# Optimization experiments

Hardware: AMD Instinct MI355X
Metric: run time of the kernel (lower is better)

Reference implementation:

```python
import jax, jax.numpy as jnp
import numpy as np

K_SCHEDULE = (4, 8, 16)


def setup_inputs() -> dict:
    key = jax.random.key(0)
    B, T, D = 2, 2048, 1024
    R = len(K_SCHEDULE)
    kx, = jax.random.split(key, 1)
    return {
        "x": jax.random.normal(kx, (B, T, D), dtype=jnp.float32),
        "gain": jnp.ones((R, D), dtype=jnp.float32),
        "bias": jnp.zeros((R, D), dtype=jnp.float32),
        "log_mix": jnp.zeros((R,), dtype=jnp.float32),
        "log_momentum": jnp.asarray(1.0, dtype=jnp.float32),
        "log_scale": jnp.asarray(0.0, dtype=jnp.float32),
    }


def _round(h, K, gain_r, bias_r, mix, momentum):
    B, T, D = h.shape
    # causal top-K adjacency from evolving hidden state
    scores = jnp.einsum("bid,bjd->bij", h, h)                      # (B,T,T)
    causal = jnp.tril(jnp.ones((T, T), dtype=bool))                # j <= i
    masked = jnp.where(causal[None], scores, -jnp.inf)
    vals, idx = jax.lax.top_k(masked, K)                           # (B,T,K)
    valid = jnp.isfinite(vals)                                     # early rows have < K causal neighbors
    # unweighted (mean) neighbor aggregation via gather
    gathered = jnp.take_along_axis(h[:, None, :, :], idx[..., None], axis=2)  # (B,T,K,D)
    vf = valid.astype(h.dtype)
    count = jnp.maximum(vf.sum(-1, keepdims=True), 1.0)            # (B,T,1)
    msg = (gathered * vf[..., None]).sum(axis=2) / count           # (B,T,D)
    # gated residual blend + affine + GELU + momentum update
    blended = mix * h + (1.0 - mix) * msg
    h_new = jax.nn.gelu(blended * gain_r + bias_r, approximate=False)
    return momentum * h + (1.0 - momentum) * h_new


def reference(x, gain, bias, log_mix, log_momentum, log_scale):
    momentum = jax.nn.sigmoid(log_momentum)
    scale = jax.nn.softplus(log_scale) + 0.01
    h = x
    for r, K_r in enumerate(K_SCHEDULE):
        mix = jax.nn.sigmoid(log_mix[r])
        h = _round(h, K_r, gain[r], bias[r], mix, momentum)
    return (h - x) * scale
```

## Files before the change

kernel.cpp:

```cpp
#include <hip/hip_runtime.h>
#include <math.h>

#define BB 2
#define TT 2048
#define DD 1024
#define NTHREADS 256

#define RT 64
#define CT 128
#define DC 32
#define NCHUNK (DD / DC)
#define NJC (TT / CT)
#define KMAX 16
#define CST 132
#define NTILES 272
#define NROWS (BB * TT)
#define CSLAB ((uint32_t)(NROWS * DC))
#define PLANE ((uint32_t)(BB * TT * DD))
#define HBUF 12288


typedef _Float16 half8  __attribute__((ext_vector_type(8)));
typedef _Float16 half4v __attribute__((ext_vector_type(4)));
typedef float    float4v __attribute__((ext_vector_type(4)));

#define GLD16(gp, lp) __builtin_amdgcn_global_load_lds(                         \
    (const __attribute__((address_space(1))) unsigned int*)(gp),                \
    (__attribute__((address_space(3))) unsigned int*)(lp), 16, 0, 0)

__device__ __forceinline__ float gelu_exact(float t) {
    return 0.5f * t * (1.0f + erff(t * 0.70710678118654752f));
}

__global__ __launch_bounds__(NTHREADS) void split_kernel(
    const float* __restrict__ h,
    _Float16* __restrict__ hiP,
    _Float16* __restrict__ loP)
{
    const int idx = blockIdx.x * NTHREADS + threadIdx.x;
    const float4 v = ((const float4*)h)[idx];
    const float xs[4] = {v.x, v.y, v.z, v.w};
    half4v hi, lo;
    #pragma unroll
    for (int u = 0; u < 4; ++u) {
        const _Float16 hh = (_Float16)xs[u];
        hi[u] = hh;
        lo[u] = (_Float16)(xs[u] - (float)hh);
    }
    const uint32_t tot  = (uint32_t)idx * 4u;
    const uint32_t grow = tot >> 10;
    const uint32_t wh   = tot & 1023u;
    const uint32_t off  = ((wh >> 5) * (uint32_t)NROWS + grow) * 32u + (wh & 31u);
    *(half4v*)(hiP + off) = hi;
    *(half4v*)(loP + off) = lo;
}

__global__ __launch_bounds__(NTHREADS) void score_topk_kernel(
    const _Float16* __restrict__ hiP,
    float* __restrict__ pval,
    int*   __restrict__ pidx,
    int K)
{
    __shared__ __align__(16) char smem_raw[49152];
    _Float16* sm  = (_Float16*)smem_raw;
    float* scores = (float*)smem_raw;

    const int b = blockIdx.y;
    const int p = blockIdx.x;
    int g = (int)(0.5f * (sqrtf(4.0f * (float)p + 1.0f) - 1.0f));
    while ((g + 1) * (g + 2) <= p) ++g;
    while (g * (g + 1) > p) --g;
    const int qq = p - g * (g + 1);
    const int it = 2 * g + qq / (g + 1);
    const int jc = qq % (g + 1);
    const int i0 = it * RT, j0 = jc * CT;

    const int tid  = threadIdx.x;
    const int lane = tid & 63, wave = tid >> 6;
    const int wr = wave & 1, wc = wave >> 1;

    uint32_t goff[6];
    #pragma unroll
    for (int slot = 0; slot < 6; ++slot) {
        const int gr = tid + NTHREADS * slot;
        int n, row; uint32_t pl;
        if (gr < 256)       { n = gr;        pl = 0; row = i0 + 16 * (n >> 6) + (n & 15); }
        else if (gr < 512)  { n = gr - 256;  pl = 1; row = i0 + 16 * (n >> 6) + (n & 15); }
        else if (gr < 1024) { n = gr - 512;  pl = 0; row = j0 + 16 * (n >> 6) + (n & 15); }
        else                { n = gr - 1024; pl = 1; row = j0 + 16 * (n >> 6) + (n & 15); }
        const int oct = (n >> 4) & 3;
        goff[slot] = pl * PLANE + (uint32_t)(b * TT + row) * DC + (uint32_t)oct * 8;
    }

    float4v acc[2][4];
    #pragma unroll
    for (int rb = 0; rb < 2; ++rb)
        #pragma unroll
        for (int cb = 0; cb < 4; ++cb)
            acc[rb][cb] = (float4v){0.f, 0.f, 0.f, 0.f};

    #pragma unroll
    for (int t = 0; t < 6; ++t)
        GLD16(hiP + goff[t], &sm[(size_t)(tid + NTHREADS * t) * 8]);
    #pragma unroll
    for (int t = 0; t < 6; ++t)
        GLD16(hiP + goff[t] + CSLAB, &sm[HBUF + (size_t)(tid + NTHREADS * t) * 8]);

    for (int c = 0; c < NCHUNK; ++c) {
        const int cur = (c & 1) ? HBUF : 0;

        if (c < NCHUNK - 1) asm volatile("s_waitcnt vmcnt(6)" ::: "memory");
        else                asm volatile("s_waitcnt vmcnt(0)" ::: "memory");
        __builtin_amdgcn_s_barrier();
        asm volatile("" ::: "memory");

        half8 ah[2], al[2], bh[4], bl[4];
        #pragma unroll
        for (int rb = 0; rb < 2; ++rb) {
            const int band = 2 * wr + rb;
            ah[rb] = *(const half8*)&sm[cur +        (band * 64 + lane) * 8];
            al[rb] = *(const half8*)&sm[cur + 2048 + (band * 64 + lane) * 8];
        }
        #pragma unroll
        for (int cb = 0; cb < 4; ++cb) {
            const int band = 4 * wc + cb;
            bh[cb] = *(const half8*)&sm[cur + 4096 + (band * 64 + lane) * 8];
            bl[cb] = *(const half8*)&sm[cur + 8192 + (band * 64 + lane) * 8];
        }

        asm volatile("s_waitcnt lgkmcnt(0)" ::: "memory");
        __builtin_amdgcn_s_barrier();
        asm volatile("" ::: "memory");

        if (c + 2 < NCHUNK) {
            #pragma unroll
            for (int t = 0; t < 6; ++t)
                GLD16(hiP + goff[t] + (uint32_t)(c + 2) * CSLAB,
                      &sm[cur + (size_t)(tid + NTHREADS * t) * 8]);
        }
        __builtin_amdgcn_sched_barrier(0);

        __builtin_amdgcn_s_setprio(1);
        #pragma unroll
        for (int rb = 0; rb < 2; ++rb)
            #pragma unroll
            for (int cb = 0; cb < 4; ++cb) {
                acc[rb][cb] = __builtin_amdgcn_mfma_f32_16x16x32_f16(ah[rb], bh[cb], acc[rb][cb], 0, 0, 0);
                acc[rb][cb] = __builtin_amdgcn_mfma_f32_16x16x32_f16(ah[rb], bl[cb], acc[rb][cb], 0, 0, 0);
                acc[rb][cb] = __builtin_amdgcn_mfma_f32_16x16x32_f16(al[rb], bh[cb], acc[rb][cb], 0, 0, 0);
            }
        __builtin_amdgcn_s_setprio(0);
    }

    {
        const int qn = lane >> 4, rn = lane & 15;
        #pragma unroll
        for (int rb = 0; rb < 2; ++rb)
            #pragma unroll
            for (int cb = 0; cb < 4; ++cb)
                #pragma unroll
                for (int reg = 0; reg < 4; ++reg) {
                    const int i_loc = 32 * wr + 16 * rb + qn * 4 + reg;
                    const int j_loc = 64 * wc + 16 * cb + rn;
                    scores[i_loc * CST + j_loc] =
                        (j0 + j_loc <= i0 + i_loc) ? acc[rb][cb][reg] : -INFINITY;
                }
    }
    __syncthreads();

    const int rloc = tid >> 2, seg = tid & 3;
    const float* Crow = scores + rloc * CST;
    float vals[32];
    #pragma unroll
    for (int cc = 0; cc < 32; ++cc) vals[cc] = Crow[seg + 4 * cc];

    uint32_t dead = 0;
    const int irow = i0 + rloc;
    const size_t obase = ((size_t)(b * TT + irow) * NJC + jc) * KMAX;
    for (int k = 0; k < K; ++k) {
        float bv = -INFINITY; int bcc = -1;
        #pragma unroll
        for (int cc = 0; cc < 32; ++cc) {
            const bool alive = ((dead >> cc) & 1u) == 0u;
            if (alive && vals[cc] > bv) { bv = vals[cc]; bcc = cc; }
        }
        const int bcol = (bcc >= 0) ? (seg + 4 * bcc) : -1;
        float wv = bv; int wcol = bcol;
        #pragma unroll
        for (int m = 1; m < 4; m <<= 1) {
            const float ov = __shfl_xor(wv, m, 64);
            const int   oc = __shfl_xor(wcol, m, 64);
            if (ov > wv || (ov == wv && (unsigned)oc < (unsigned)wcol)) { wv = ov; wcol = oc; }
        }
        if (seg == 0) {
            pval[obase + k] = wv;
            pidx[obase + k] = (wcol >= 0) ? (j0 + wcol) : -1;
        }
        if (bcc >= 0 && wcol == bcol) dead |= (1u << bcc);
    }
}

template<int K>
__global__ __launch_bounds__(NTHREADS) void merge_agg_kernel(
    const float* __restrict__ h_in,
    float* __restrict__ h_out,
    const float* __restrict__ pval,
    const int*   __restrict__ pidx,
    const float* __restrict__ gain,
    const float* __restrict__ bias,
    const float* __restrict__ log_mix_r,
    const float* __restrict__ log_momentum,
    const float* __restrict__ xres,
    const float* __restrict__ log_scale,
    _Float16* __restrict__ hiO,
    _Float16* __restrict__ loO)
{
    constexpr int KL = (K == 4) ? 2 : (K == 8) ? 3 : 4;
    __shared__ __align__(16) float s_cval[NTHREADS];
    __shared__ __align__(16) int   s_cidx[NTHREADS];
    __shared__ int s_sel[KMAX];

    const int row = blockIdx.x, b = row / TT, i = row % TT;
    const int tid = threadIdx.x;
    const float* hb = h_in + (size_t)b * TT * DD;

    const int count = (i + 1 < K) ? (i + 1) : K;
    const int jcn = i / CT + 1;
    const int ncand = jcn * K;

    float mv = -INFINITY; int mj = -1;
    if (tid < ncand) {
        const int w = tid >> KL, k = tid & (K - 1);
        const size_t base = ((size_t)(b * TT + i) * NJC + w) * KMAX + k;
        const int j = pidx[base];
        if (j >= 0) { mj = j; mv = pval[base]; }
    }
    s_cval[tid] = mv;
    s_cidx[tid] = mj;

    const float4 hi = ((const float4*)(hb + (size_t)i * DD))[tid];
    const float4 g4 = ((const float4*)gain)[tid];
    const float4 c4 = ((const float4*)bias)[tid];
    __syncthreads();

    if (mj >= 0) {
        const int nb = (ncand + 3) >> 2;
        int rank = 0;
        for (int q = 0; q < nb; ++q) {
            const float4 v4 = ((const float4*)s_cval)[q];
            const int4  j4 = ((const int4*)s_cidx)[q];
            rank += (v4.x > mv || (v4.x == mv && (unsigned)j4.x < (unsigned)mj));
            rank += (v4.y > mv || (v4.y == mv && (unsigned)j4.y < (unsigned)mj));
            rank += (v4.z > mv || (v4.z == mv && (unsigned)j4.z < (unsigned)mj));
            rank += (v4.w > mv || (v4.w == mv && (unsigned)j4.w < (unsigned)mj));
        }
        if (rank < count) s_sel[rank] = mj;
    }
    __syncthreads();

    const float mix      = 1.0f / (1.0f + expf(-log_mix_r[0]));
    const float momentum = 1.0f / (1.0f + expf(-log_momentum[0]));
    const float inv_cnt  = 1.0f / (float)count;

    float4 msg = make_float4(0.f, 0.f, 0.f, 0.f);
    if (count == K) {
        #pragma unroll
        for (int k = 0; k < K; ++k) {
            const float4 v = ((const float4*)(hb + (size_t)s_sel[k] * DD))[tid];
            msg.x += v.x; msg.y += v.y; msg.z += v.z; msg.w += v.w;
        }
    } else {
        for (int k = 0; k < count; ++k) {
            const float4 v = ((const float4*)(hb + (size_t)s_sel[k] * DD))[tid];
            msg.x += v.x; msg.y += v.y; msg.z += v.z; msg.w += v.w;
        }
    }

    float4 o;
    {
        float m, t;
        m = msg.x * inv_cnt; t = (mix * hi.x + (1.f - mix) * m) * g4.x + c4.x;
        o.x = momentum * hi.x + (1.f - momentum) * gelu_exact(t);
        m = msg.y * inv_cnt; t = (mix * hi.y + (1.f - mix) * m) * g4.y + c4.y;
        o.y = momentum * hi.y + (1.f - momentum) * gelu_exact(t);
        m = msg.z * inv_cnt; t = (mix * hi.z + (1.f - mix) * m) * g4.z + c4.z;
        o.z = momentum * hi.z + (1.f - momentum) * gelu_exact(t);
        m = msg.w * inv_cnt; t = (mix * hi.w + (1.f - mix) * m) * g4.w + c4.w;
        o.w = momentum * hi.w + (1.f - momentum) * gelu_exact(t);
    }

    if (hiO != nullptr) {
        const float os[4] = {o.x, o.y, o.z, o.w};
        half4v hv, lv;
        #pragma unroll
        for (int u = 0; u < 4; ++u) {
            const _Float16 hh = (_Float16)os[u];
            hv[u] = hh;
            lv[u] = (_Float16)(os[u] - (float)hh);
        }
        const uint32_t wh  = (uint32_t)tid * 4u;
        const uint32_t off = ((wh >> 5) * (uint32_t)NROWS + (uint32_t)row) * 32u + (wh & 31u);
        *(half4v*)(hiO + off) = hv;
        *(half4v*)(loO + off) = lv;
    }

    if (xres != nullptr) {
        const float scale = log1pf(expf(log_scale[0])) + 0.01f;
        const float4 xv = ((const float4*)(xres + (size_t)row * DD))[tid];
        o.x = (o.x - xv.x) * scale;
        o.y = (o.y - xv.y) * scale;
        o.z = (o.z - xv.z) * scale;
        o.w = (o.w - xv.w) * scale;
    }
    ((float4*)(h_out + (size_t)row * DD))[tid] = o;
}

extern "C" void kernel_launch(void* const* d_in, const int* in_sizes, int n_in,
                              void* d_out, int out_size, void* d_ws, size_t ws_size,
                              hipStream_t stream) {
    const float* x            = (const float*)d_in[0];
    const float* gain         = (const float*)d_in[1];
    const float* bias         = (const float*)d_in[2];
    const float* log_mix      = (const float*)d_in[3];
    const float* log_momentum = (const float*)d_in[4];
    const float* log_scale    = (const float*)d_in[5];
    float* out = (float*)d_out;

    char* wsb = (char*)d_ws;
    float*     h_ws = (float*)wsb;
    float*     pval = (float*)(wsb + (size_t)BB * TT * DD * 4);
    int*       pidx = (int*)  (wsb + (size_t)BB * TT * DD * 4 + (size_t)BB * TT * NJC * KMAX * 4);
    _Float16*  hiP  = (_Float16*)(wsb + (size_t)BB * TT * DD * 4 + (size_t)BB * TT * NJC * KMAX * 8);
    _Float16*  loP  = hiP + (size_t)PLANE;

    const dim3 sgrid(NTILES, BB);
    const int nsplit = BB * TT * DD / 4 / NTHREADS;

    split_kernel<<<nsplit, NTHREADS, 0, stream>>>(x, hiP, loP);
    score_topk_kernel<<<sgrid, NTHREADS, 0, stream>>>(hiP, pval, pidx, 4);
    merge_agg_kernel<4><<<BB * TT, NTHREADS, 0, stream>>>(
        x, out, pval, pidx, gain + 0 * DD, bias + 0 * DD, log_mix + 0, log_momentum,
        nullptr, nullptr, hiP, loP);
    score_topk_kernel<<<sgrid, NTHREADS, 0, stream>>>(hiP, pval, pidx, 8);
    merge_agg_kernel<8><<<BB * TT, NTHREADS, 0, stream>>>(
        out, h_ws, pval, pidx, gain + 1 * DD, bias + 1 * DD, log_mix + 1, log_momentum,
        nullptr, nullptr, hiP, loP);
    score_topk_kernel<<<sgrid, NTHREADS, 0, stream>>>(hiP, pval, pidx, 16);
    merge_agg_kernel<16><<<BB * TT, NTHREADS, 0, stream>>>(
        h_ws, out, pval, pidx, gain + 2 * DD, bias + 2 * DD, log_mix + 2, log_momentum,
        x, log_scale, nullptr, nullptr);
}
```

Baseline: 301.0 us.

## Triple-buffer LDS chunks in score kernel to drop one barrier per chunk

Switches the score GEMM's LDS staging from two buffers to three and unrolls the chunk loop by three. The prefetch for chunk c+2 can then go into a third buffer right after the first barrier, which removes the second per-chunk barrier that used to protect buffer reuse. In exchange, LDS use grows from 48KB to 72KB per block, which may cut the number of resident blocks per CU and so reduce occupancy. A final syncthreads is added before the scores reuse the shared memory.

```diff
diff --git a/kernel.cpp b/kernel.cpp
--- a/kernel.cpp
+++ b/kernel.cpp
@@ -17,7 +17,9 @@
 #define NROWS (BB * TT)
 #define CSLAB ((uint32_t)(NROWS * DC))
 #define PLANE ((uint32_t)(BB * TT * DD))
-#define HBUF 12288
+#define B0 0
+#define B1 12288
+#define B2 24576
 
 
 typedef _Float16 half8  __attribute__((ext_vector_type(8)));
@@ -61,7 +63,7 @@
     int*   __restrict__ pidx,
     int K)
 {
-    __shared__ __align__(16) char smem_raw[49152];
+    __shared__ __align__(16) char smem_raw[73728];
     _Float16* sm  = (_Float16*)smem_raw;
     float* scores = (float*)smem_raw;
 
@@ -101,56 +103,62 @@
 
     #pragma unroll
     for (int t = 0; t < 6; ++t)
-        GLD16(hiP + goff[t], &sm[(size_t)(tid + NTHREADS * t) * 8]);
+        GLD16(hiP + goff[t], &sm[B0 + (size_t)(tid + NTHREADS * t) * 8]);
     #pragma unroll
     for (int t = 0; t < 6; ++t)
-        GLD16(hiP + goff[t] + CSLAB, &sm[HBUF + (size_t)(tid + NTHREADS * t) * 8]);
-
-    for (int c = 0; c < NCHUNK; ++c) {
-        const int cur = (c & 1) ? HBUF : 0;
-
-        if (c < NCHUNK - 1) asm volatile("s_waitcnt vmcnt(6)" ::: "memory");
-        else                asm volatile("s_waitcnt vmcnt(0)" ::: "memory");
-        __builtin_amdgcn_s_barrier();
-        asm volatile("" ::: "memory");
-
-        half8 ah[2], al[2], bh[4], bl[4];
-        #pragma unroll
-        for (int rb = 0; rb < 2; ++rb) {
-            const int band = 2 * wr + rb;
-            ah[rb] = *(const half8*)&sm[cur +        (band * 64 + lane) * 8];
-            al[rb] = *(const half8*)&sm[cur + 2048 + (band * 64 + lane) * 8];
-        }
-        #pragma unroll
-        for (int cb = 0; cb < 4; ++cb) {
-            const int band = 4 * wc + cb;
-            bh[cb] = *(const half8*)&sm[cur + 4096 + (band * 64 + lane) * 8];
-            bl[cb] = *(const half8*)&sm[cur + 8192 + (band * 64 + lane) * 8];
-        }
-
-        asm volatile("s_waitcnt lgkmcnt(0)" ::: "memory");
-        __builtin_amdgcn_s_barrier();
-        asm volatile("" ::: "memory");
-
-        if (c + 2 < NCHUNK) {
-            #pragma unroll
-            for (int t = 0; t < 6; ++t)
-                GLD16(hiP + goff[t] + (uint32_t)(c + 2) * CSLAB,
-                      &sm[cur + (size_t)(tid + NTHREADS * t) * 8]);
-        }
-        __builtin_amdgcn_sched_barrier(0);
-
-        __builtin_amdgcn_s_setprio(1);
-        #pragma unroll
-        for (int rb = 0; rb < 2; ++rb)
-            #pragma unroll
-            for (int cb = 0; cb < 4; ++cb) {
-                acc[rb][cb] = __builtin_amdgcn_mfma_f32_16x16x32_f16(ah[rb], bh[cb], acc[rb][cb], 0, 0, 0);
-                acc[rb][cb] = __builtin_amdgcn_mfma_f32_16x16x32_f16(ah[rb], bl[cb], acc[rb][cb], 0, 0, 0);
-                acc[rb][cb] = __builtin_amdgcn_mfma_f32_16x16x32_f16(al[rb], bh[cb], acc[rb][cb], 0, 0, 0);
-            }
-        __builtin_amdgcn_s_setprio(0);
-    }
+        GLD16(hiP + goff[t] + CSLAB, &sm[B1 + (size_t)(tid + NTHREADS * t) * 8]);
+
+#define CHUNK1B(c, BCUR, BNXT, VMSTR, DO_ISSUE) do {                              \
+        asm volatile("s_waitcnt vmcnt(" VMSTR ")" ::: "memory");                  \
+        __builtin_amdgcn_s_barrier();                                             \
+        asm volatile("" ::: "memory");                                            \
+        if (DO_ISSUE) {                                                           \
+            _Pragma("unroll")                                                     \
+            for (int t = 0; t < 6; ++t)                                           \
+                GLD16(hiP + goff[t] + (uint32_t)((c) + 2) * CSLAB,                \
+                      &sm[(BNXT) + (size_t)(tid + NTHREADS * t) * 8]);            \
+        }                                                                         \
+        __builtin_amdgcn_sched_barrier(0);                                        \
+        half8 ah[2], al[2], bh[4], bl[4];                                         \
+        _Pragma("unroll")                                                         \
+        for (int rb = 0; rb < 2; ++rb) {                                          \
+            const int band = 2 * wr + rb;                                         \
+            ah[rb] = *(const half8*)&sm[(BCUR) +        (band * 64 + lane) * 8];  \
+            al[rb] = *(const half8*)&sm[(BCUR) + 2048 + (band * 64 + lane) * 8];  \
+        }                                                                         \
+        _Pragma("unroll")                                                         \
+        for (int cb = 0; cb < 4; ++cb) {                                          \
+            const int band = 4 * wc + cb;                                         \
+            bh[cb] = *(const half8*)&sm[(BCUR) + 4096 + (band * 64 + lane) * 8];  \
+            bl[cb] = *(const half8*)&sm[(BCUR) + 8192 + (band * 64 + lane) * 8];  \
+        }                                                                         \
+        asm volatile("s_waitcnt lgkmcnt(0)" ::: "memory");                        \
+        __builtin_amdgcn_sched_barrier(0);                                        \
+        __builtin_amdgcn_s_setprio(1);                                            \
+        _Pragma("unroll")                                                         \
+        for (int rb = 0; rb < 2; ++rb)                                            \
+            _Pragma("unroll")                                                     \
+            for (int cb = 0; cb < 4; ++cb) {                                      \
+                acc[rb][cb] = __builtin_amdgcn_mfma_f32_16x16x32_f16(             \
+                    ah[rb], bh[cb], acc[rb][cb], 0, 0, 0);                        \
+                acc[rb][cb] = __builtin_amdgcn_mfma_f32_16x16x32_f16(             \
+                    ah[rb], bl[cb], acc[rb][cb], 0, 0, 0);                        \
+                acc[rb][cb] = __builtin_amdgcn_mfma_f32_16x16x32_f16(             \
+                    al[rb], bh[cb], acc[rb][cb], 0, 0, 0);                        \
+            }                                                                     \
+        __builtin_amdgcn_s_setprio(0);                                            \
+    } while (0)
+
+    for (int ct = 0; ct < 10; ++ct) {
+        CHUNK1B(3 * ct + 0, B0, B2, "6", 1);
+        CHUNK1B(3 * ct + 1, B1, B0, "6", 1);
+        CHUNK1B(3 * ct + 2, B2, B1, "6", 1);
+    }
+    CHUNK1B(30, B0, B2, "6", 0);
+    CHUNK1B(31, B1, B0, "0", 0);
+#undef CHUNK1B
+
+    __syncthreads();
 
     {
         const int qn = lane >> 4, rn = lane & 15;
```

New measurement: 311.2 us. 1.03x slower.

## Software-pipeline LDS fragment loads against MFMA with register double-buffering

Applied to the files above, without the earlier changes.

Restructures the score GEMM main loop so that the LDS fragments for the next K-chunk are read into a second register set while the MFMAs for the current chunk run. This needs only one barrier per chunk instead of two. The loop is unrolled by two with explicit even and odd fragment sets. Launch bounds now request 3 blocks per CU to cap register use. The doubled fragment registers plus the occupancy hint risk spills, and the wait is now vmcnt(0) each step instead of vmcnt(6), which can expose global load latency.

```diff
diff --git a/kernel.cpp b/kernel.cpp
--- a/kernel.cpp
+++ b/kernel.cpp
@@ -55,7 +55,7 @@
     *(half4v*)(loP + off) = lo;
 }
 
-__global__ __launch_bounds__(NTHREADS) void score_topk_kernel(
+__global__ __launch_bounds__(NTHREADS, 3) void score_topk_kernel(
     const _Float16* __restrict__ hiP,
     float* __restrict__ pval,
     int*   __restrict__ pidx,
@@ -99,58 +99,85 @@
         for (int cb = 0; cb < 4; ++cb)
             acc[rb][cb] = (float4v){0.f, 0.f, 0.f, 0.f};
 
+    half8 ahE[2], alE[2], bhE[4], blE[4];
+    half8 ahO[2], alO[2], bhO[4], blO[4];
+
+#define LDFRAG(AH, AL, BH, BL, BASE) do {                                        \
+        _Pragma("unroll")                                                        \
+        for (int rb = 0; rb < 2; ++rb) {                                         \
+            const int band = 2 * wr + rb;                                        \
+            AH[rb] = *(const half8*)&sm[(BASE) +        (band * 64 + lane) * 8]; \
+            AL[rb] = *(const half8*)&sm[(BASE) + 2048 + (band * 64 + lane) * 8]; \
+        }                                                                        \
+        _Pragma("unroll")                                                        \
+        for (int cb = 0; cb < 4; ++cb) {                                         \
+            const int band = 4 * wc + cb;                                        \
+            BH[cb] = *(const half8*)&sm[(BASE) + 4096 + (band * 64 + lane) * 8]; \
+            BL[cb] = *(const half8*)&sm[(BASE) + 8192 + (band * 64 + lane) * 8]; \
+        }                                                                        \
+    } while (0)
+
+#define DOMFMA(AH, AL, BH, BL) do {                                              \
+        __builtin_amdgcn_s_setprio(1);                                           \
+        _Pragma("unroll")                                                        \
+        for (int rb = 0; rb < 2; ++rb)                                           \
+            _Pragma("unroll")                                                    \
+            for (int cb = 0; cb < 4; ++cb) {                                     \
+                acc[rb][cb] = __builtin_amdgcn_mfma_f32_16x16x32_f16(            \
+                    AH[rb], BH[cb], acc[rb][cb], 0, 0, 0);                       \
+                acc[rb][cb] = __builtin_amdgcn_mfma_f32_16x16x32_f16(            \
+                    AH[rb], BL[cb], acc[rb][cb], 0, 0, 0);                       \
+                acc[rb][cb] = __builtin_amdgcn_mfma_f32_16x16x32_f16(            \
+                    AL[rb], BH[cb], acc[rb][cb], 0, 0, 0);                       \
+            }                                                                    \
+        __builtin_amdgcn_s_setprio(0);                                           \
+    } while (0)
+
+#define PIPE(BCUR, BNXT, FaH, FaL, FbH, FbL, NaH, NaL, NbH, NbL, DO_DMA)         \
+    do {                                                                         \
+        asm volatile("s_waitcnt lgkmcnt(0)" ::: "memory");                       \
+        asm volatile("s_waitcnt vmcnt(0)"  ::: "memory");                        \
+        __builtin_amdgcn_s_barrier();                                            \
+        __builtin_amdgcn_sched_barrier(0);                                       \
+        if (DO_DMA) {                                                            \
+            _Pragma("unroll")                                                    \
+            for (int t = 0; t < 6; ++t)                                          \
+                GLD16(hiP + goff[t] + coff,                                      \
+                      &sm[(BCUR) + (size_t)(tid + NTHREADS * t) * 8]);           \
+            coff += (uint32_t)CSLAB;                                             \
+        }                                                                        \
+        __builtin_amdgcn_sched_barrier(0);                                       \
+        LDFRAG(NaH, NaL, NbH, NbL, BNXT);                                        \
+        __builtin_amdgcn_sched_barrier(0);                                       \
+        DOMFMA(FaH, FaL, FbH, FbL);                                              \
+    } while (0)
+
     #pragma unroll
     for (int t = 0; t < 6; ++t)
         GLD16(hiP + goff[t], &sm[(size_t)(tid + NTHREADS * t) * 8]);
     #pragma unroll
     for (int t = 0; t < 6; ++t)
         GLD16(hiP + goff[t] + CSLAB, &sm[HBUF + (size_t)(tid + NTHREADS * t) * 8]);
-
-    for (int c = 0; c < NCHUNK; ++c) {
-        const int cur = (c & 1) ? HBUF : 0;
-
-        if (c < NCHUNK - 1) asm volatile("s_waitcnt vmcnt(6)" ::: "memory");
-        else                asm volatile("s_waitcnt vmcnt(0)" ::: "memory");
-        __builtin_amdgcn_s_barrier();
-        asm volatile("" ::: "memory");
-
-        half8 ah[2], al[2], bh[4], bl[4];
-        #pragma unroll
-        for (int rb = 0; rb < 2; ++rb) {
-            const int band = 2 * wr + rb;
-            ah[rb] = *(const half8*)&sm[cur +        (band * 64 + lane) * 8];
-            al[rb] = *(const half8*)&sm[cur + 2048 + (band * 64 + lane) * 8];
-        }
-        #pragma unroll
-        for (int cb = 0; cb < 4; ++cb) {
-            const int band = 4 * wc + cb;
-            bh[cb] = *(const half8*)&sm[cur + 4096 + (band * 64 + lane) * 8];
-            bl[cb] = *(const half8*)&sm[cur + 8192 + (band * 64 + lane) * 8];
-        }
-
-        asm volatile("s_waitcnt lgkmcnt(0)" ::: "memory");
-        __builtin_amdgcn_s_barrier();
-        asm volatile("" ::: "memory");
-
-        if (c + 2 < NCHUNK) {
-            #pragma unroll
-            for (int t = 0; t < 6; ++t)
-                GLD16(hiP + goff[t] + (uint32_t)(c + 2) * CSLAB,
-                      &sm[cur + (size_t)(tid + NTHREADS * t) * 8]);
-        }
-        __builtin_amdgcn_sched_barrier(0);
-
-        __builtin_amdgcn_s_setprio(1);
-        #pragma unroll
-        for (int rb = 0; rb < 2; ++rb)
-            #pragma unroll
-            for (int cb = 0; cb < 4; ++cb) {
-                acc[rb][cb] = __builtin_amdgcn_mfma_f32_16x16x32_f16(ah[rb], bh[cb], acc[rb][cb], 0, 0, 0);
-                acc[rb][cb] = __builtin_amdgcn_mfma_f32_16x16x32_f16(ah[rb], bl[cb], acc[rb][cb], 0, 0, 0);
-                acc[rb][cb] = __builtin_amdgcn_mfma_f32_16x16x32_f16(al[rb], bh[cb], acc[rb][cb], 0, 0, 0);
-            }
-        __builtin_amdgcn_s_setprio(0);
-    }
+    asm volatile("s_waitcnt vmcnt(6)" ::: "memory");
+    __builtin_amdgcn_s_barrier();
+    asm volatile("" ::: "memory");
+    LDFRAG(ahE, alE, bhE, blE, 0);
+
+    uint32_t coff = 2u * CSLAB;
+
+    for (int ci = 0; ci < 15; ++ci) {
+        PIPE(0,    HBUF, ahE, alE, bhE, blE, ahO, alO, bhO, blO, 1);
+        PIPE(HBUF, 0,    ahO, alO, bhO, blO, ahE, alE, bhE, blE, 1);
+    }
+    PIPE(0, HBUF, ahE, alE, bhE, blE, ahO, alO, bhO, blO, 0);
+    asm volatile("s_waitcnt lgkmcnt(0)" ::: "memory");
+    __builtin_amdgcn_sched_barrier(0);
+    DOMFMA(ahO, alO, bhO, blO);
+#undef PIPE
+#undef DOMFMA
+#undef LDFRAG
+
+    __syncthreads();
 
     {
         const int qn = lane >> 4, rn = lane & 15;
```

Result: no change. 296.3 us (-1.6%).

## Enlarge score tile to 128x128 with 512-thread blocks

Applied to the files above, without the earlier changes.

The score/top-k kernel now computes square 128x128 tiles of the causal score matrix using 8 waves per block instead of 64x128 tiles with 4 waves. The triangular tile enumeration changes to match, and per-block shared memory grows. The goal is more reuse of each loaded fragment and fewer blocks with redundant loads. In exchange there are fewer, larger blocks, possibly lower occupancy, and more wasted work on diagonal tiles. The top-k epilogue, unchanged in the visible code, must handle 128 score rows with 512 threads.

```diff
diff --git a/kernel.cpp b/kernel.cpp
--- a/kernel.cpp
+++ b/kernel.cpp
@@ -4,20 +4,21 @@
 #define BB 2
 #define TT 2048
 #define DD 1024
-#define NTHREADS 256
-
-#define RT 64
+
+#define RT 128
 #define CT 128
 #define DC 32
 #define NCHUNK (DD / DC)
 #define NJC (TT / CT)
 #define KMAX 16
 #define CST 132
-#define NTILES 272
+#define NT2 136
 #define NROWS (BB * TT)
 #define CSLAB ((uint32_t)(NROWS * DC))
 #define PLANE ((uint32_t)(BB * TT * DD))
-#define HBUF 12288
+#define HBUF 16384
+#define NTH_S 512
+#define NTHREADS 256
 
 
 typedef _Float16 half8  __attribute__((ext_vector_type(8)));
@@ -55,77 +56,75 @@
     *(half4v*)(loP + off) = lo;
 }
 
-__global__ __launch_bounds__(NTHREADS) void score_topk_kernel(
+__global__ __launch_bounds__(NTH_S) void score_topk_kernel(
     const _Float16* __restrict__ hiP,
     float* __restrict__ pval,
     int*   __restrict__ pidx,
     int K)
 {
-    __shared__ __align__(16) char smem_raw[49152];
+    __shared__ __align__(16) char smem_raw[67584];
     _Float16* sm  = (_Float16*)smem_raw;
     float* scores = (float*)smem_raw;
 
     const int b = blockIdx.y;
     const int p = blockIdx.x;
-    int g = (int)(0.5f * (sqrtf(4.0f * (float)p + 1.0f) - 1.0f));
-    while ((g + 1) * (g + 2) <= p) ++g;
-    while (g * (g + 1) > p) --g;
-    const int qq = p - g * (g + 1);
-    const int it = 2 * g + qq / (g + 1);
-    const int jc = qq % (g + 1);
+    int it = (int)((sqrtf(8.0f * (float)p + 1.0f) - 1.0f) * 0.5f);
+    while ((it + 1) * (it + 2) / 2 <= p) ++it;
+    while (it * (it + 1) / 2 > p) --it;
+    const int jc = p - it * (it + 1) / 2;
     const int i0 = it * RT, j0 = jc * CT;
 
     const int tid  = threadIdx.x;
     const int lane = tid & 63, wave = tid >> 6;
     const int wr = wave & 1, wc = wave >> 1;
 
-    uint32_t goff[6];
-    #pragma unroll
-    for (int slot = 0; slot < 6; ++slot) {
-        const int gr = tid + NTHREADS * slot;
-        int n, row; uint32_t pl;
-        if (gr < 256)       { n = gr;        pl = 0; row = i0 + 16 * (n >> 6) + (n & 15); }
-        else if (gr < 512)  { n = gr - 256;  pl = 1; row = i0 + 16 * (n >> 6) + (n & 15); }
-        else if (gr < 1024) { n = gr - 512;  pl = 0; row = j0 + 16 * (n >> 6) + (n & 15); }
-        else                { n = gr - 1024; pl = 1; row = j0 + 16 * (n >> 6) + (n & 15); }
+    uint32_t goff[4];
+    #pragma unroll
+    for (int slot = 0; slot < 4; ++slot) {
+        const int gr = tid + NTH_S * slot;
+        const int region = gr >> 9;
+        const int n = gr & 511;
+        const uint32_t pl = (uint32_t)(region & 1);
+        const int row0 = (region < 2) ? i0 : j0;
+        const int row = row0 + 16 * (n >> 6) + (n & 15);
         const int oct = (n >> 4) & 3;
         goff[slot] = pl * PLANE + (uint32_t)(b * TT + row) * DC + (uint32_t)oct * 8;
     }
 
-    float4v acc[2][4];
-    #pragma unroll
-    for (int rb = 0; rb < 2; ++rb)
-        #pragma unroll
-        for (int cb = 0; cb < 4; ++cb)
+    float4v acc[4][2];
+    #pragma unroll
+    for (int rb = 0; rb < 4; ++rb)
+        #pragma unroll
+        for (int cb = 0; cb < 2; ++cb)
             acc[rb][cb] = (float4v){0.f, 0.f, 0.f, 0.f};
 
     #pragma unroll
-    for (int t = 0; t < 6; ++t)
-        GLD16(hiP + goff[t], &sm[(size_t)(tid + NTHREADS * t) * 8]);
-    #pragma unroll
-    for (int t = 0; t < 6; ++t)
-        GLD16(hiP + goff[t] + CSLAB, &sm[HBUF + (size_t)(tid + NTHREADS * t) * 8]);
+    for (int t = 0; t < 4; ++t)
+        GLD16(hiP + goff[t], &sm[(size_t)(tid + NTH_S * t) * 8]);
+    #pragma unroll
+    for (int t = 0; t < 4; ++t)
+        GLD16(hiP + goff[t] + CSLAB, &sm[HBUF + (size_t)(tid + NTH_S * t) * 8]);
 
     for (int c = 0; c < NCHUNK; ++c) {
         const int cur = (c & 1) ? HBUF : 0;
 
-        if (c < NCHUNK - 1) asm volatile("s_waitcnt vmcnt(6)" ::: "memory");
+        if (c < NCHUNK - 1) asm volatile("s_waitcnt vmcnt(4)" ::: "memory");
         else                asm volatile("s_waitcnt vmcnt(0)" ::: "memory");
         __builtin_amdgcn_s_barrier();
         asm volatile("" ::: "memory");
 
-        half8 ah[2], al[2], bh[4], bl[4];
-        #pragma unroll
-        for (int rb = 0; rb < 2; ++rb) {
-            const int band = 2 * wr + rb;
+        half8 ah[4], al[4], bh[2], bl[2];
+        #pragma unroll
+        for (int rb = 0; rb < 4; ++rb) {
+            const int band = 4 * wr + rb;
             ah[rb] = *(const half8*)&sm[cur +        (band * 64 + lane) * 8];
-            al[rb] = *(const half8*)&sm[cur + 2048 + (band * 64 + lane) * 8];
-        }
-        #pragma unroll
-        for (int cb = 0; cb < 4; ++cb) {
-            const int band = 4 * wc + cb;
-            bh[cb] = *(const half8*)&sm[cur + 4096 + (band * 64 + lane) * 8];
-            bl[cb] = *(const half8*)&sm[cur + 8192 + (band * 64 + lane) * 8];
+            al[rb] = *(const half8*)&sm[cur + 4096 + (band * 64 + lane) * 8];
+        }
+        #pragma unroll
+        for (int cb = 0; cb < 2; ++cb) {
+            const int band = 2 * wc + cb;
+            bh[cb] = *(const half8*)&sm[cur +  8192 + (band * 64 + lane) * 8];
+            bl[cb] = *(const half8*)&sm[cur + 12288 + (band * 64 + lane) * 8];
         }
 
         asm volatile("s_waitcnt lgkmcnt(0)" ::: "memory");
@@ -134,17 +133,17 @@
 
         if (c + 2 < NCHUNK) {
             #pragma unroll
-            for (int t = 0; t < 6; ++t)
+            for (int t = 0; t < 4; ++t)
                 GLD16(hiP + goff[t] + (uint32_t)(c + 2) * CSLAB,
-                      &sm[cur + (size_t)(tid + NTHREADS * t) * 8]);
+                      &sm[cur + (size_t)(tid + NTH_S * t) * 8]);
         }
         __builtin_amdgcn_sched_barrier(0);
 
         __builtin_amdgcn_s_setprio(1);
         #pragma unroll
-        for (int rb = 0; rb < 2; ++rb)
+        for (int rb = 0; rb < 4; ++rb)
             #pragma unroll
-            for (int cb = 0; cb < 4; ++cb) {
+            for (int cb = 0; cb < 2; ++cb) {
                 acc[rb][cb] = __builtin_amdgcn_mfma_f32_16x16x32_f16(ah[rb], bh[cb], acc[rb][cb], 0, 0, 0);
                 acc[rb][cb] = __builtin_amdgcn_mfma_f32_16x16x32_f16(ah[rb], bl[cb], acc[rb][cb], 0, 0, 0);
                 acc[rb][cb] = __builtin_amdgcn_mfma_f32_16x16x32_f16(al[rb], bh[cb], acc[rb][cb], 0, 0, 0);
@@ -152,16 +151,18 @@
         __builtin_amdgcn_s_setprio(0);
     }
 
+    __syncthreads();
+
     {
         const int qn = lane >> 4, rn = lane & 15;
         #pragma unroll
-        for (int rb = 0; rb < 2; ++rb)
+        for (int rb = 0; rb < 4; ++rb)
             #pragma unroll
-            for (int cb = 0; cb < 4; ++cb)
+            for (int cb = 0; cb < 2; ++cb)
                 #pragma unroll
                 for (int reg = 0; reg < 4; ++reg) {
-                    const int i_loc = 32 * wr + 16 * rb + qn * 4 + reg;
-                    const int j_loc = 64 * wc + 16 * cb + rn;
+                    const int i_loc = 64 * wr + 16 * rb + qn * 4 + reg;
+                    const int j_loc = 32 * wc + 16 * cb + rn;
                     scores[i_loc * CST + j_loc] =
                         (j0 + j_loc <= i0 + i_loc) ? acc[rb][cb][reg] : -INFINITY;
                 }
@@ -333,19 +334,19 @@
     _Float16*  hiP  = (_Float16*)(wsb + (size_t)BB * TT * DD * 4 + (size_t)BB * TT * NJC * KMAX * 8);
     _Float16*  loP  = hiP + (size_t)PLANE;
 
-    const dim3 sgrid(NTILES, BB);
+    const dim3 sgrid(NT2, BB);
     const int nsplit = BB * TT * DD / 4 / NTHREADS;
 
     split_kernel<<<nsplit, NTHREADS, 0, stream>>>(x, hiP, loP);
-    score_topk_kernel<<<sgrid, NTHREADS, 0, stream>>>(hiP, pval, pidx, 4);
+    score_topk_kernel<<<sgrid, NTH_S, 0, stream>>>(hiP, pval, pidx, 4);
     merge_agg_kernel<4><<<BB * TT, NTHREADS, 0, stream>>>(
         x, out, pval, pidx, gain + 0 * DD, bias + 0 * DD, log_mix + 0, log_momentum,
         nullptr, nullptr, hiP, loP);
-    score_topk_kernel<<<sgrid, NTHREADS, 0, stream>>>(hiP, pval, pidx, 8);
+    score_topk_kernel<<<sgrid, NTH_S, 0, stream>>>(hiP, pval, pidx, 8);
     merge_agg_kernel<8><<<BB * TT, NTHREADS, 0, stream>>>(
         out, h_ws, pval, pidx, gain + 1 * DD, bias + 1 * DD, log_mix + 1, log_momentum,
         nullptr, nullptr, hiP, loP);
-    score_topk_kernel<<<sgrid, NTHREADS, 0, stream>>>(hiP, pval, pidx, 16);
+    score_topk_kernel<<<sgrid, NTH_S, 0, stream>>>(hiP, pval, pidx, 16);
     merge_agg_kernel<16><<<BB * TT, NTHREADS, 0, stream>>>(
         h_ws, out, pval, pidx, gain + 2 * DD, bias + 2 * DD, log_mix + 2, log_momentum,
         x, log_scale, nullptr, nullptr);
```

New measurement: 301.6 us. No clear change (+0.2%).
